# Kernel tuning notes

Hardware: AMD Instinct MI355X
Metric: run time of the kernel (lower is better)

Reference implementation:

```python
import math
import jax, jax.numpy as jnp
import numpy as np

B, T, C, H = 4, 2048, 1024, 16
D = C // H  # head dim = 64


def setup_inputs() -> dict:
    key = jax.random.key(0)
    ks = jax.random.split(key, 9)
    s = 1.0 / math.sqrt(C)
    return {
        "x": jax.random.normal(ks[0], (B, T, C), jnp.float32),
        "Wq": jax.random.normal(ks[1], (C, C), jnp.float32) * s,
        "bq": jax.random.normal(ks[2], (C,), jnp.float32) * 0.02,
        "Wk": jax.random.normal(ks[3], (C, C), jnp.float32) * s,
        "bk": jax.random.normal(ks[4], (C,), jnp.float32) * 0.02,
        "Wv": jax.random.normal(ks[5], (C, C), jnp.float32) * s,
        "bv": jax.random.normal(ks[6], (C,), jnp.float32) * 0.02,
        "Wo": jax.random.normal(ks[7], (C, C), jnp.float32) * s,
        "bo": jax.random.normal(ks[8], (C,), jnp.float32) * 0.02,
    }


def reference(x, Wq, bq, Wk, bk, Wv, bv, Wo, bo):
    # Projections: (B,T,C) -> (B,H,T,D)
    def heads(y):
        return y.reshape(B, T, H, D).transpose(0, 2, 1, 3)

    q = heads(x @ Wq + bq)
    k = heads(x @ Wk + bk)
    v = heads(x @ Wv + bv)

    scale = 1.0 / math.sqrt(D)
    scores = jnp.einsum("bhqd,bhkd->bhqk", q, k) * scale  # (B,H,T,T)
    causal = jnp.tril(jnp.ones((T, T), dtype=bool))
    scores = jnp.where(causal[None, None], scores, jnp.float32(-jnp.inf))
    att = jax.nn.softmax(scores, axis=-1)

    y = jnp.einsum("bhqk,bhkd->bhqd", att, v)  # (B,H,T,D)
    y = y.transpose(0, 2, 1, 3).reshape(B, T, C)
    return y @ Wo + bo
```

## Files before the change

kernel.cpp:

```cpp
#include <hip/hip_runtime.h>

#define B_ 4
#define T_ 2048
#define C_ 1024
#define H_ 16
#define D_ 64
#define M_ (B_*T_)
#define CR3 3072

typedef unsigned short u16;
typedef __attribute__((ext_vector_type(8))) short short8;
typedef __attribute__((ext_vector_type(8))) unsigned short ushort8_t;
typedef __attribute__((ext_vector_type(4))) unsigned short ushort4_t;
typedef __attribute__((ext_vector_type(4))) float floatx4;
typedef __attribute__((ext_vector_type(16))) float f32x16;
typedef __attribute__((ext_vector_type(4))) unsigned int uint4_t;

__device__ __forceinline__ u16 f2bf(float f) {
  union { float f; unsigned u; } v; v.f = f;
  unsigned r = v.u + 0x7fffu + ((v.u >> 16) & 1u);
  return (u16)(r >> 16);
}

__device__ __forceinline__ void gload16(const void* g, void* l) {
  __builtin_amdgcn_global_load_lds((__attribute__((address_space(1))) void*)(g),
                                   (__attribute__((address_space(3))) void*)(l),
                                   16, 0, 0);
}

__device__ __forceinline__ unsigned cvtpk(float lo, float hi) {
  unsigned r;
  asm("v_cvt_pk_bf16_f32 %0, %1, %2" : "=v"(r) : "v"(lo), "v"(hi));
  return r;
}

__device__ __forceinline__ void pl32swap(unsigned &a, unsigned &b) {
  asm volatile("v_permlane32_swap_b32 %0, %1" : "+v"(a), "+v"(b));
}

#define MFMA32(a, b, c) __builtin_amdgcn_mfma_f32_32x32x16_bf16(a, b, c, 0, 0, 0)
#define MFMA16(a, b, c) __builtin_amdgcn_mfma_f32_16x16x32_bf16(a, b, c, 0, 0, 0)

__global__ __launch_bounds__(256) void convx_k(const float* __restrict__ x,
                                               u16* __restrict__ o) {
  int i = (blockIdx.x * 256 + threadIdx.x) * 4;
  floatx4 v = *(const floatx4*)(x + i);
  ushort4_t r;
#pragma unroll
  for (int j = 0; j < 4; ++j) r[j] = f2bf(v[j]);
  *(ushort4_t*)(o + i) = r;
}

__global__ __launch_bounds__(256) void wconv_k(const float* __restrict__ W0,
                                               const float* __restrict__ W1,
                                               const float* __restrict__ W2,
                                               const float* __restrict__ W3,
                                               u16* __restrict__ WT) {
  __shared__ float tile[64][65];
  const float* W = blockIdx.z == 0 ? W0 : blockIdx.z == 1 ? W1 : blockIdx.z == 2 ? W2 : W3;
  const float sc = blockIdx.z == 0 ? 0.125f * 1.44269504f : 1.0f;
  u16* Wt = WT + (size_t)blockIdx.z * (C_ * C_);
  int k0 = blockIdx.x * 64, n0 = blockIdx.y * 64;
  int t = threadIdx.x;
  int r = t >> 2, c0 = (t & 3) * 16;
#pragma unroll
  for (int j = 0; j < 4; ++j) {
    floatx4 v = *(const floatx4*)(W + (size_t)(k0 + r) * C_ + n0 + c0 + j * 4);
#pragma unroll
    for (int jj = 0; jj < 4; ++jj) tile[r][c0 + j * 4 + jj] = v[jj];
  }
  __syncthreads();
  ushort8_t o0, o1;
#pragma unroll
  for (int j = 0; j < 8; ++j) o0[j] = f2bf(tile[c0 + j][r] * sc);
#pragma unroll
  for (int j = 0; j < 8; ++j) o1[j] = f2bf(tile[c0 + 8 + j][r] * sc);
  *(ushort8_t*)(Wt + (size_t)(n0 + r) * C_ + k0 + c0) = o0;
  *(ushort8_t*)(Wt + (size_t)(n0 + r) * C_ + k0 + c0 + 8) = o1;
}

__global__ __launch_bounds__(512, 2) void gemm8_k(const u16* __restrict__ A,
                                                  const u16* __restrict__ Wt,
                                                  const float* __restrict__ b0,
                                                  const float* __restrict__ b1,
                                                  const float* __restrict__ b2,
                                                  float bsc0,
                                                  u16* __restrict__ Cout) {
  __shared__ u16 lds[65536];
  const int tid = threadIdx.x;
  const int lane = tid & 63, w = tid >> 6;
  const int wm = w >> 2, wn = w & 3;
  const int l15 = lane & 15, g = lane >> 4;
  const int swl = (l15 & 7) << 3;

  const int nwg = gridDim.x, cpx = nwg >> 3, bid = blockIdx.x;
  const int swz = (bid & 7) * cpx + (bid >> 3);
  const int bm = swz & 31, bn = swz >> 5;
  const int m0 = bm * 256, n0 = bn * 256;

  const int srow = tid >> 3;
  const int scol = ((tid & 7) ^ (srow & 7)) * 8;
  const u16* gA = A + (size_t)(m0 + srow) * 1024 + scol;
  const u16* gB = Wt + (size_t)(n0 + srow) * 1024 + scol;

#define STAGE8(KT, BUF) do { \
    u16* la_ = lds + (BUF) * 32768 + tid * 8; \
    const u16* pa_ = gA + (KT) * 64; \
    const u16* pb_ = gB + (KT) * 64; \
    gload16(pa_, la_);                 gload16(pa_ + 64 * 1024, la_ + 4096); \
    gload16(pa_ + 128 * 1024, la_ + 8192); gload16(pa_ + 192 * 1024, la_ + 12288); \
    gload16(pb_, la_ + 16384);         gload16(pb_ + 64 * 1024, la_ + 20480); \
    gload16(pb_ + 128 * 1024, la_ + 24576); gload16(pb_ + 192 * 1024, la_ + 28672); \
  } while (0)

  floatx4 acc[8][4] = {};

  STAGE8(0, 0);
  STAGE8(1, 1);
  asm volatile("s_waitcnt vmcnt(8)" ::: "memory");
  __syncthreads();

  for (int t = 0; t < 16; ++t) {
    const u16* Ab = lds + (t & 1) * 32768;
    const u16* Bb = Ab + 16384;
    short8 bfr[4][2];
#pragma unroll
    for (int ni = 0; ni < 4; ++ni)
#pragma unroll
      for (int ks = 0; ks < 2; ++ks)
        bfr[ni][ks] = *(const short8*)(Bb + (wn * 64 + ni * 16 + l15) * 64 +
                                       ((ks * 32 + g * 8) ^ swl));
#pragma unroll
    for (int mh = 0; mh < 2; ++mh) {
      short8 af[4][2];
#pragma unroll
      for (int mi = 0; mi < 4; ++mi)
#pragma unroll
        for (int ks = 0; ks < 2; ++ks)
          af[mi][ks] = *(const short8*)(Ab + (wm * 128 + mh * 64 + mi * 16 + l15) * 64 +
                                        ((ks * 32 + g * 8) ^ swl));
      __builtin_amdgcn_s_setprio(1);
#pragma unroll
      for (int mi = 0; mi < 4; ++mi)
#pragma unroll
        for (int ni = 0; ni < 4; ++ni)
#pragma unroll
          for (int ks = 0; ks < 2; ++ks)
            acc[mh * 4 + mi][ni] = MFMA16(af[mi][ks], bfr[ni][ks], acc[mh * 4 + mi][ni]);
      __builtin_amdgcn_s_setprio(0);
    }
    __syncthreads();
    if (t + 2 < 16) {
      STAGE8(t + 2, t & 1);
      asm volatile("s_waitcnt vmcnt(8)" ::: "memory");
      __syncthreads();
    } else if (t == 14) {
      asm volatile("s_waitcnt vmcnt(0)" ::: "memory");
      __syncthreads();
    }
  }

#pragma unroll
  for (int mi8 = 0; mi8 < 8; ++mi8) {
    int row = m0 + wm * 128 + (mi8 >> 2) * 64 + (mi8 & 3) * 16 + g * 4;
#pragma unroll
    for (int ni = 0; ni < 4; ++ni) {
      int col = n0 + wn * 64 + ni * 16 + l15;
      int seg = col >> 10;
      const float* bp = seg == 0 ? b0 : seg == 1 ? b1 : b2;
      float bv = bp[col & 1023] * (seg == 0 ? bsc0 : 1.0f);
#pragma unroll
      for (int i = 0; i < 4; ++i)
        Cout[(size_t)(row + i) * CR3 + col] = f2bf(acc[mi8][ni][i] + bv);
    }
  }
}

template <int OUTF32>
__global__ __launch_bounds__(256, 2) void gemm_k(const u16* __restrict__ A,
                                                 const u16* __restrict__ Wt,
                                                 const float* __restrict__ b0,
                                                 void* __restrict__ Cout, int ostride) {
  __shared__ u16 As[128 * 32];
  __shared__ u16 Bs[128 * 32];
  const int tid = threadIdx.x;
  const int w = tid >> 6, lane = tid & 63;
  const int wr = (w >> 1) * 64, wc = (w & 1) * 64;
  const int l15 = lane & 15, g = lane >> 4;
  const int m0 = blockIdx.x * 128, n0 = blockIdx.y * 128;

  floatx4 acc[4][4] = {};

  const u16* ga = A + (size_t)(m0 + (tid >> 2)) * C_ + (tid & 3) * 8;
  const u16* gb = Wt + (size_t)(n0 + (tid >> 2)) * C_ + (tid & 3) * 8;
  u16* lA = As + tid * 8;
  u16* lB = Bs + tid * 8;

  for (int kt = 0; kt < C_; kt += 32) {
    gload16(ga + kt, lA);
    gload16(ga + kt + (size_t)64 * C_, lA + 64 * 32);
    gload16(gb + kt, lB);
    gload16(gb + kt + (size_t)64 * C_, lB + 64 * 32);
    asm volatile("s_waitcnt vmcnt(0)" ::: "memory");
    __syncthreads();
    short8 af[4], bf[4];
#pragma unroll
    for (int i = 0; i < 4; ++i)
      af[i] = *(const short8*)(As + (wr + i * 16 + l15) * 32 + g * 8);
#pragma unroll
    for (int i = 0; i < 4; ++i)
      bf[i] = *(const short8*)(Bs + (wc + i * 16 + l15) * 32 + g * 8);
#pragma unroll
    for (int mi = 0; mi < 4; ++mi)
#pragma unroll
      for (int ni = 0; ni < 4; ++ni)
        acc[mi][ni] = MFMA16(af[mi], bf[ni], acc[mi][ni]);
    __syncthreads();
  }
#pragma unroll
  for (int mi = 0; mi < 4; ++mi) {
    int row = m0 + wr + mi * 16 + g * 4;
#pragma unroll
    for (int ni = 0; ni < 4; ++ni) {
      int col = n0 + wc + ni * 16 + l15;
      float bv = b0[col];
#pragma unroll
      for (int i = 0; i < 4; ++i) {
        float v = acc[mi][ni][i] + bv;
        if (OUTF32)
          ((float*)Cout)[(size_t)(row + i) * ostride + col] = v;
        else
          ((u16*)Cout)[(size_t)(row + i) * ostride + col] = f2bf(v);
      }
    }
  }
}

__global__ __launch_bounds__(256, 2) void attn_k(const u16* __restrict__ QKV,
                                                 u16* __restrict__ Yg) {
  __shared__ u16 Ks[2][64 * 64];
  __shared__ u16 Vt[2][64 * 64];

  const int tid = threadIdx.x;
  const int w = tid >> 6, lane = tid & 63;
  const int qi = lane & 31, h = lane >> 5;

  const int lid = blockIdx.x;
  const int a4 = lid >> 6;
  const int gq = a4 >> 2, iq = a4 & 3;
  const int jt = gq == 0 ? 15 - 2 * iq : gq == 1 ? 2 * iq : gq == 2 ? 14 - 2 * iq : 1 + 2 * iq;
  const int bh = lid & 63;
  const int nt = 2 * jt + 2;

  const size_t baseQ = (size_t)(bh >> 4) * T_ * CR3 + (size_t)(bh & 15) * D_;
  const size_t baseY = (size_t)(bh >> 4) * T_ * C_ + (size_t)(bh & 15) * D_;
  const u16* Kg = QKV + baseQ + 1024;
  const u16* Vg = QKV + baseQ + 2048;

  const int srow = tid >> 3, schunk = tid & 7;
  const int sgcol = (schunk ^ (srow & 7)) * 8;
  const u16* Kgr = Kg + (size_t)srow * CR3 + sgcol;
  const u16* Vgr = Vg + (size_t)srow * CR3 + schunk * 8;

  const int qw0 = 128 * jt + 32 * w;
  const int q_abs = qw0 + qi;

  short8 qf0, qf1, qf2, qf3;
  {
    const u16* Qr = QKV + baseQ + (size_t)q_abs * CR3 + 8 * h;
    qf0 = *(const short8*)(Qr);      qf1 = *(const short8*)(Qr + 16);
    qf2 = *(const short8*)(Qr + 32); qf3 = *(const short8*)(Qr + 48);
  }

  ushort8_t va, vbr;
  gload16(Kgr, &Ks[0][tid * 8]);
  gload16(Kgr + (size_t)32 * CR3, &Ks[0][2048 + tid * 8]);
  va = *(const ushort8_t*)(Vgr);
  vbr = *(const ushort8_t*)(Vgr + (size_t)32 * CR3);

  f32x16 y0 = {}, y1 = {};
  float l_run = 0.f;
  const float M0 = 13.0f;

  for (int t = 0; t < nt; ++t) {
    const int kv0 = t * 64;
    u16* Kb = Ks[t & 1];
    u16* Vb = Vt[t & 1];
    asm volatile("s_waitcnt vmcnt(0)" ::: "memory");
    {
      char* vbp = (char*)Vb;
#pragma unroll
      for (int j = 0; j < 8; ++j) {
        int d = schunk * 8 + j;
        int sl = ((schunk ^ j) & 7) << 4;
        *(u16*)(vbp + d * 128 + ((2 * srow) ^ sl)) = va[j];
        *(u16*)(vbp + d * 128 + ((2 * (srow + 32)) ^ sl)) = vbr[j];
      }
    }
    __syncthreads();
    if (t + 1 < nt) {
      int nkv = (t + 1) * 64;
      u16* dst = Ks[(t + 1) & 1];
      gload16(Kgr + (size_t)nkv * CR3, dst + tid * 8);
      gload16(Kgr + (size_t)(nkv + 32) * CR3, dst + 2048 + tid * 8);
      va = *(const ushort8_t*)(Vgr + (size_t)nkv * CR3);
      vbr = *(const ushort8_t*)(Vgr + (size_t)(nkv + 32) * CR3);
    }

    if (kv0 <= qw0 + 31) {
      f32x16 s0 = {}, s1 = {};
      {
        const int swq = (qi & 7) << 4;
        const char* kr0 = (const char*)Kb + qi * 128;
        const char* kr1 = (const char*)Kb + (qi + 32) * 128;
        short8 k0, k1;
        k0 = *(const short8*)(kr0 + ((16 * h) ^ swq));
        k1 = *(const short8*)(kr1 + ((16 * h) ^ swq));
        s0 = MFMA32(k0, qf0, s0); s1 = MFMA32(k1, qf0, s1);
        k0 = *(const short8*)(kr0 + ((32 + 16 * h) ^ swq));
        k1 = *(const short8*)(kr1 + ((32 + 16 * h) ^ swq));
        s0 = MFMA32(k0, qf1, s0); s1 = MFMA32(k1, qf1, s1);
        k0 = *(const short8*)(kr0 + ((64 + 16 * h) ^ swq));
        k1 = *(const short8*)(kr1 + ((64 + 16 * h) ^ swq));
        s0 = MFMA32(k0, qf2, s0); s1 = MFMA32(k1, qf2, s1);
        k0 = *(const short8*)(kr0 + ((96 + 16 * h) ^ swq));
        k1 = *(const short8*)(kr1 + ((96 + 16 * h) ^ swq));
        s0 = MFMA32(k0, qf3, s0); s1 = MFMA32(k1, qf3, s1);
      }
      if (kv0 + 63 > qw0) {
#pragma unroll
        for (int r = 0; r < 16; ++r) {
          int kvq = (r & 3) + 8 * (r >> 2) + 4 * h;
          if (kv0 + kvq > q_abs) s0[r] = -1e30f;
          if (kv0 + 32 + kvq > q_abs) s1[r] = -1e30f;
        }
      }
#pragma unroll
      for (int r = 0; r < 16; ++r) s0[r] = __builtin_amdgcn_exp2f(s0[r] - M0);
#pragma unroll
      for (int r = 0; r < 16; ++r) s1[r] = __builtin_amdgcn_exp2f(s1[r] - M0);
      {
        float a8[8];
#pragma unroll
        for (int r = 0; r < 8; ++r) a8[r] = (s0[r] + s0[r + 8]) + (s1[r] + s1[r + 8]);
#pragma unroll
        for (int r = 0; r < 4; ++r) a8[r] += a8[r + 4];
        l_run += (a8[0] + a8[1]) + (a8[2] + a8[3]);
      }
      unsigned pw[16];
      {
        unsigned a0, b0, a1, b1;
        a0 = cvtpk(s0[0], s0[1]);  b0 = cvtpk(s0[4], s0[5]);  pl32swap(a0, b0);
        a1 = cvtpk(s0[2], s0[3]);  b1 = cvtpk(s0[6], s0[7]);  pl32swap(a1, b1);
        pw[0] = a0; pw[1] = a1; pw[2] = b0; pw[3] = b1;
        a0 = cvtpk(s0[8], s0[9]);  b0 = cvtpk(s0[12], s0[13]); pl32swap(a0, b0);
        a1 = cvtpk(s0[10], s0[11]); b1 = cvtpk(s0[14], s0[15]); pl32swap(a1, b1);
        pw[4] = a0; pw[5] = a1; pw[6] = b0; pw[7] = b1;
        a0 = cvtpk(s1[0], s1[1]);  b0 = cvtpk(s1[4], s1[5]);  pl32swap(a0, b0);
        a1 = cvtpk(s1[2], s1[3]);  b1 = cvtpk(s1[6], s1[7]);  pl32swap(a1, b1);
        pw[8] = a0; pw[9] = a1; pw[10] = b0; pw[11] = b1;
        a0 = cvtpk(s1[8], s1[9]);  b0 = cvtpk(s1[12], s1[13]); pl32swap(a0, b0);
        a1 = cvtpk(s1[10], s1[11]); b1 = cvtpk(s1[14], s1[15]); pl32swap(a1, b1);
        pw[12] = a0; pw[13] = a1; pw[14] = b0; pw[15] = b1;
      }
      {
        const char* vb0 = (const char*)Vb + qi * 128;
        const char* vb1 = (const char*)Vb + (qi + 32) * 128;
        const int sx0 = (((qi >> 3) ^ qi) & 7) << 4;
        const int sx1 = sx0 ^ 0x40;
#pragma unroll
        for (int c = 0; c < 4; ++c) {
          int cb = 32 * c + 16 * h;
          uint4_t pt = {pw[c * 4 + 0], pw[c * 4 + 1], pw[c * 4 + 2], pw[c * 4 + 3]};
          short8 pa = __builtin_bit_cast(short8, pt);
          short8 v0 = *(const short8*)(vb0 + (cb ^ sx0));
          short8 v1 = *(const short8*)(vb1 + (cb ^ sx1));
          y0 = MFMA32(pa, v0, y0);
          y1 = MFMA32(pa, v1, y1);
        }
      }
    }
    __syncthreads();
  }

  l_run += __shfl_xor(l_run, 32);
  float linv = 1.0f / l_run;
#pragma unroll
  for (int r = 0; r < 16; ++r) {
    int qp = (r & 3) + 8 * (r >> 2) + 4 * h;
    float lv = __shfl(linv, qp);
    size_t row = baseY + (size_t)(qw0 + qp) * C_;
    Yg[row + qi] = f2bf(y0[r] * lv);
    Yg[row + 32 + qi] = f2bf(y1[r] * lv);
  }
}

extern "C" void kernel_launch(void* const* d_in, const int* in_sizes, int n_in,
                              void* d_out, int out_size, void* d_ws, size_t ws_size,
                              hipStream_t stream) {
  const float* x  = (const float*)d_in[0];
  const float* Wq = (const float*)d_in[1];
  const float* bq = (const float*)d_in[2];
  const float* Wk = (const float*)d_in[3];
  const float* bk = (const float*)d_in[4];
  const float* Wv = (const float*)d_in[5];
  const float* bv = (const float*)d_in[6];
  const float* Wo = (const float*)d_in[7];
  const float* bo = (const float*)d_in[8];
  float* out = (float*)d_out;

  char* ws = (char*)d_ws;
  u16* xb   = (u16*)ws;
  u16* WT   = (u16*)(ws + (size_t)16777216);
  u16* QKVb = (u16*)(ws + (size_t)25165824);
  u16* Yb = xb;

  convx_k<<<dim3(M_ * C_ / 1024), 256, 0, stream>>>(x, xb);
  wconv_k<<<dim3(16, 16, 4), 256, 0, stream>>>(Wq, Wk, Wv, Wo, WT);
  gemm8_k<<<dim3(384), 512, 0, stream>>>(xb, WT, bq, bk, bv, 0.125f * 1.44269504f, QKVb);
  attn_k<<<dim3(1024), 256, 0, stream>>>(QKVb, Yb);
  gemm_k<1><<<dim3(64, 8), 256, 0, stream>>>(Yb, WT + (size_t)3 * 1048576, bo, out, C_);
}
```

Baseline: 188.1 us.

## Rework QKV GEMM into a 4-stage LDS ring with K-tile 32

Restructures the fused QKV projection GEMM from a double-buffered K-tile of 64 with two barriers per step into a four-slot LDS ring. Each slot holds a K-tile of 32, is prefetched two tiles ahead and needs only one barrier per iteration. Global loads for A and B are split around the two MFMA halves so memory traffic overlaps with compute, and the LDS swizzle is adapted to 32-wide rows. The block-swizzle divisor is hardcoded to the grid size. This trades more loop iterations and smaller per-barrier work for fewer synchronisations and finer-grained overlap.

```diff
diff --git a/kernel.cpp b/kernel.cpp
--- a/kernel.cpp
+++ b/kernel.cpp
@@ -86,94 +86,100 @@
                                                   const float* __restrict__ b2,
                                                   float bsc0,
                                                   u16* __restrict__ Cout) {
-  __shared__ u16 lds[65536];
+  __shared__ u16 lds4[65536];
   const int tid = threadIdx.x;
   const int lane = tid & 63, w = tid >> 6;
   const int wm = w >> 2, wn = w & 3;
   const int l15 = lane & 15, g = lane >> 4;
-  const int swl = (l15 & 7) << 3;
-
-  const int nwg = gridDim.x, cpx = nwg >> 3, bid = blockIdx.x;
-  const int swz = (bid & 7) * cpx + (bid >> 3);
+
+  const int bid = blockIdx.x;
+  const int swz = (bid & 7) * 48 + (bid >> 3);
   const int bm = swz & 31, bn = swz >> 5;
   const int m0 = bm * 256, n0 = bn * 256;
 
-  const int srow = tid >> 3;
-  const int scol = ((tid & 7) ^ (srow & 7)) * 8;
-  const u16* gA = A + (size_t)(m0 + srow) * 1024 + scol;
-  const u16* gB = Wt + (size_t)(n0 + srow) * 1024 + scol;
-
-#define STAGE8(KT, BUF) do { \
-    u16* la_ = lds + (BUF) * 32768 + tid * 8; \
-    const u16* pa_ = gA + (KT) * 64; \
-    const u16* pb_ = gB + (KT) * 64; \
-    gload16(pa_, la_);                 gload16(pa_ + 64 * 1024, la_ + 4096); \
-    gload16(pa_ + 128 * 1024, la_ + 8192); gload16(pa_ + 192 * 1024, la_ + 12288); \
-    gload16(pb_, la_ + 16384);         gload16(pb_ + 64 * 1024, la_ + 20480); \
-    gload16(pb_ + 128 * 1024, la_ + 24576); gload16(pb_ + 192 * 1024, la_ + 28672); \
-  } while (0)
+  const int i1 = w * 128 + lane, i2 = i1 + 64;
+  const int r1 = i1 >> 2, c1 = ((i1 & 3) ^ (r1 & 3)) << 3;
+  const int r2 = i2 >> 2, c2 = ((i2 & 3) ^ (r2 & 3)) << 3;
+  const u16* gA1 = A + (size_t)(m0 + r1) * 1024 + c1;
+  const u16* gA2 = A + (size_t)(m0 + r2) * 1024 + c2;
+  const u16* gB1 = Wt + (size_t)(n0 + r1) * 1024 + c1;
+  const u16* gB2 = Wt + (size_t)(n0 + r2) * 1024 + c2;
 
   floatx4 acc[8][4] = {};
 
-  STAGE8(0, 0);
-  STAGE8(1, 1);
-  asm volatile("s_waitcnt vmcnt(8)" ::: "memory");
-  __syncthreads();
-
-  for (int t = 0; t < 16; ++t) {
-    const u16* Ab = lds + (t & 1) * 32768;
-    const u16* Bb = Ab + 16384;
-    short8 bfr[4][2];
-#pragma unroll
-    for (int ni = 0; ni < 4; ++ni)
-#pragma unroll
-      for (int ks = 0; ks < 2; ++ks)
-        bfr[ni][ks] = *(const short8*)(Bb + (wn * 64 + ni * 16 + l15) * 64 +
-                                       ((ks * 32 + g * 8) ^ swl));
-#pragma unroll
-    for (int mh = 0; mh < 2; ++mh) {
-      short8 af[4][2];
-#pragma unroll
-      for (int mi = 0; mi < 4; ++mi)
-#pragma unroll
-        for (int ks = 0; ks < 2; ++ks)
-          af[mi][ks] = *(const short8*)(Ab + (wm * 128 + mh * 64 + mi * 16 + l15) * 64 +
-                                        ((ks * 32 + g * 8) ^ swl));
-      __builtin_amdgcn_s_setprio(1);
-#pragma unroll
-      for (int mi = 0; mi < 4; ++mi)
-#pragma unroll
-        for (int ni = 0; ni < 4; ++ni)
-#pragma unroll
-          for (int ks = 0; ks < 2; ++ks)
-            acc[mh * 4 + mi][ni] = MFMA16(af[mi][ks], bfr[ni][ks], acc[mh * 4 + mi][ni]);
-      __builtin_amdgcn_s_setprio(0);
-    }
-    __syncthreads();
-    if (t + 2 < 16) {
-      STAGE8(t + 2, t & 1);
-      asm volatile("s_waitcnt vmcnt(8)" ::: "memory");
-      __syncthreads();
-    } else if (t == 14) {
-      asm volatile("s_waitcnt vmcnt(0)" ::: "memory");
-      __syncthreads();
-    }
-  }
-
-#pragma unroll
-  for (int mi8 = 0; mi8 < 8; ++mi8) {
-    int row = m0 + wm * 128 + (mi8 >> 2) * 64 + (mi8 & 3) * 16 + g * 4;
+  {
+    u16* d0 = lds4;
+    u16* d1 = lds4 + 16384;
+    gload16(gA1, d0 + i1 * 8);              gload16(gA2, d0 + i2 * 8);
+    gload16(gB1, d0 + 8192 + i1 * 8);       gload16(gB2, d0 + 8192 + i2 * 8);
+    gload16(gA1 + 32, d1 + i1 * 8);         gload16(gA2 + 32, d1 + i2 * 8);
+    gload16(gB1 + 32, d1 + 8192 + i1 * 8);  gload16(gB2 + 32, d1 + 8192 + i2 * 8);
+  }
+
+  for (int kt = 0; kt < 32; ++kt) {
+    const u16* Ab = lds4 + (kt & 3) * 16384;
+    const u16* Bb = Ab + 8192;
+    u16* ds = lds4 + ((kt + 2) & 3) * 16384;
+    if (kt < 30) {
+      gload16(gA1 + (kt + 2) * 32, ds + i1 * 8);
+      gload16(gA2 + (kt + 2) * 32, ds + i2 * 8);
+    }
+    if (kt < 30)       asm volatile("s_waitcnt vmcnt(6)" ::: "memory");
+    else if (kt == 30) asm volatile("s_waitcnt vmcnt(4)" ::: "memory");
+    else               asm volatile("s_waitcnt vmcnt(0)" ::: "memory");
+    __builtin_amdgcn_s_barrier();
+    short8 bfr[4], af[4];
 #pragma unroll
     for (int ni = 0; ni < 4; ++ni) {
-      int col = n0 + wn * 64 + ni * 16 + l15;
-      int seg = col >> 10;
-      const float* bp = seg == 0 ? b0 : seg == 1 ? b1 : b2;
-      float bv = bp[col & 1023] * (seg == 0 ? bsc0 : 1.0f);
-#pragma unroll
-      for (int i = 0; i < 4; ++i)
-        Cout[(size_t)(row + i) * CR3 + col] = f2bf(acc[mi8][ni][i] + bv);
-    }
-  }
+      int rb = wn * 64 + ni * 16 + l15;
+      bfr[ni] = *(const short8*)(Bb + rb * 32 + ((g ^ (rb & 3)) << 3));
+    }
+#pragma unroll
+    for (int mi = 0; mi < 4; ++mi) {
+      int ra = wm * 128 + mi * 16 + l15;
+      af[mi] = *(const short8*)(Ab + ra * 32 + ((g ^ (ra & 3)) << 3));
+    }
+    __builtin_amdgcn_s_setprio(1);
+#pragma unroll
+    for (int mi = 0; mi < 4; ++mi)
+#pragma unroll
+      for (int ni = 0; ni < 4; ++ni)
+        acc[mi][ni] = MFMA16(af[mi], bfr[ni], acc[mi][ni]);
+    __builtin_amdgcn_s_setprio(0);
+    if (kt < 30) {
+      gload16(gB1 + (kt + 2) * 32, ds + 8192 + i1 * 8);
+      gload16(gB2 + (kt + 2) * 32, ds + 8192 + i2 * 8);
+    }
+#pragma unroll
+    for (int mi = 0; mi < 4; ++mi) {
+      int ra = wm * 128 + 64 + mi * 16 + l15;
+      af[mi] = *(const short8*)(Ab + ra * 32 + ((g ^ (ra & 3)) << 3));
+    }
+    __builtin_amdgcn_s_setprio(1);
+#pragma unroll
+    for (int mi = 0; mi < 4; ++mi)
+#pragma unroll
+      for (int ni = 0; ni < 4; ++ni)
+        acc[4 + mi][ni] = MFMA16(af[mi], bfr[ni], acc[4 + mi][ni]);
+    __builtin_amdgcn_s_setprio(0);
+  }
+
+#pragma unroll
+  for (int s = 0; s < 2; ++s)
+#pragma unroll
+    for (int mi = 0; mi < 4; ++mi) {
+      int row = m0 + wm * 128 + s * 64 + mi * 16 + g * 4;
+#pragma unroll
+      for (int ni = 0; ni < 4; ++ni) {
+        int col = n0 + wn * 64 + ni * 16 + l15;
+        int seg = col >> 10;
+        const float* bp = seg == 0 ? b0 : seg == 1 ? b1 : b2;
+        float bv = bp[col & 1023] * (seg == 0 ? bsc0 : 1.0f);
+#pragma unroll
+        for (int i = 0; i < 4; ++i)
+          Cout[(size_t)(row + i) * CR3 + col] = f2bf(acc[s * 4 + mi][ni][i] + bv);
+      }
+    }
 }
 
 template <int OUTF32>
```

Result: faster. 168.6 us (-10.4%).
